# Optimization experiments

Hardware: AMD Instinct MI355X
Metric: run time of the kernel (lower is better)

The kernel has to match this reference:

```python
import jax, jax.numpy as jnp
import numpy as np

BATCH, IN_DIM, GRID, HID, DEPTH = 2048, 128, 128, 256, 7
BN_EPS = 1e-5


def setup_inputs() -> dict:
    key = jax.random.key(0)
    ks = jax.random.split(key, 10)
    x = jax.random.uniform(ks[0], (BATCH, IN_DIM), dtype=jnp.float32)
    grids = jax.random.uniform(ks[1], (DEPTH, IN_DIM, GRID), dtype=jnp.float32)  # torch.rand init
    fs = jax.random.normal(ks[2], (DEPTH, IN_DIM, GRID, HID), dtype=jnp.float32)
    depth_scores = jnp.ones((DEPTH,), dtype=jnp.float32)
    mlp_W = jax.random.normal(ks[3], (3, HID, HID), dtype=jnp.float32) * (1.0 / np.sqrt(HID))
    mlp_b = jnp.zeros((3, HID), dtype=jnp.float32)
    bn_gamma = jnp.ones((3, HID), dtype=jnp.float32)
    bn_beta = jnp.zeros((3, HID), dtype=jnp.float32)
    W_out = jax.random.normal(ks[4], (HID, 1), dtype=jnp.float32) * (1.0 / np.sqrt(HID))
    b_out = jnp.zeros((1,), dtype=jnp.float32)
    return {"x": x, "grids": grids, "fs": fs, "depth_scores": depth_scores,
            "mlp_W": mlp_W, "mlp_b": mlp_b, "bn_gamma": bn_gamma,
            "bn_beta": bn_beta, "W_out": W_out, "b_out": b_out}


def reference(x, grids, fs, depth_scores, mlp_W, mlp_b, bn_gamma, bn_beta, W_out, b_out):
    # per-feature min-max normalization over the batch dim
    xmin = x.min(axis=0, keepdims=True)
    xmax = x.max(axis=0, keepdims=True)
    z = (x - xmin) / (xmax - xmin + 1e-6)  # [B, I]

    outputs = []
    for i in range(DEPTH):
        Bmat = jax.nn.relu(z[:, :, None] - grids[i][None, :, :])  # [B, I, G]
        # (B.unsqueeze(-1) * fs[i]).sum(2).sum(1) == einsum big,igh->bh
        H = jnp.einsum('big,igh->bh', Bmat, fs[i])  # [B, H]
        if i > 0:  # residual accumulation
            H = H + outputs[-1]
        outputs.append(H)
    stacked = jnp.stack(outputs, axis=0)  # [D, B, H]
    w = jax.nn.softmax(depth_scores)  # depth attention
    h = jnp.einsum('d,dbh->bh', w, stacked)

    # MLP head (BatchNorm uses batch stats = training-mode behaviour; Dropout off)
    for j in range(3):
        h = h @ mlp_W[j] + mlp_b[j]
        mean = h.mean(axis=0)
        var = h.var(axis=0)  # biased, matching torch BN normalization
        h = (h - mean) * jax.lax.rsqrt(var + BN_EPS) * bn_gamma[j] + bn_beta[j]
        h = jax.nn.gelu(h, approximate=False)  # torch nn.GELU is exact erf GELU
    return h @ W_out + b_out
```

## Files before the change

kernel.cpp:

```cpp
#include <hip/hip_runtime.h>
#include <hip/hip_bf16.h>

#define BATCH 2048
#define IN_DIM 128
#define GRIDN 128
#define HID 256
#define DEPTH 7

typedef unsigned int u32;
typedef __attribute__((ext_vector_type(8))) short short8;
typedef __attribute__((ext_vector_type(4))) float floatx4;

#define OFF_FST   ((size_t)0)
#define SZ_FST    ((size_t)7*128*256*128*2)
#define OFF_ZT    (OFF_FST + SZ_FST)
#define SZ_ZT     ((size_t)BATCH*IN_DIM*4)
#define OFF_HPRE  (OFF_ZT + SZ_ZT)
#define SZ_HPRE   ((size_t)BATCH*HID*4)
#define OFF_STATS (OFF_HPRE + SZ_HPRE)
#define SZ_STATS  ((size_t)3*2*HID*4)
#define OFF_KEYS  (OFF_STATS + SZ_STATS)
#define SZ_KEYS   ((size_t)256*4)
#define OFF_CW    (OFF_KEYS + SZ_KEYS)
#define SZ_CW     ((size_t)32)
#define OFF_Y1    (OFF_CW + SZ_CW)
#define SZ_Y      ((size_t)BATCH*HID*4)
#define OFF_Y2    (OFF_Y1 + SZ_Y)
#define OFF_Y3    (OFF_Y2 + SZ_Y)

__device__ __forceinline__ void gload_lds16(const void* g, void* l) {
  __builtin_amdgcn_global_load_lds(
      (const __attribute__((address_space(1))) u32*)g,
      (__attribute__((address_space(3))) u32*)l, 16, 0, 0);
}

__device__ __forceinline__ u32 pack2_bf16(float lo, float hi) {
  __hip_bfloat162 b2;
  b2.x = __float2bfloat16(lo);
  b2.y = __float2bfloat16(hi);
  return *reinterpret_cast<u32*>(&b2);
}

__device__ __forceinline__ u32 pk_trunc(float a, float b) {
  return __builtin_amdgcn_perm(__float_as_uint(b), __float_as_uint(a), 0x07060302u);
}

__device__ __forceinline__ float gelu_exact(float x) {
  return 0.5f * x * (1.0f + erff(x * 0.70710678118654752f));
}

__global__ void prep1_kernel(const float* __restrict__ x, u32* __restrict__ keys,
                             const float* __restrict__ depth_scores,
                             float* __restrict__ cw) {
  int t = threadIdx.x;
  int base = blockIdx.x * 256 + t;
  float mn = 1e30f, mx = -1e30f;
#pragma unroll
  for (int j = 0; j < 16; ++j) {
    float v = x[base + j * 16384];
    mn = fminf(mn, v); mx = fmaxf(mx, v);
  }
  __shared__ float smn[256], smx[256];
  smn[t] = mn; smx[t] = mx;
  __syncthreads();
  if (t < 128) {
    mn = fminf(smn[t], smn[t + 128]);
    mx = fmaxf(smx[t], smx[t + 128]);
    int i = base & 127;
    atomicMax(&keys[i], 0x7FFFFFFFu - __float_as_uint(mn));
    atomicMax(&keys[128 + i], __float_as_uint(mx));
  }
  if (blockIdx.x == 0 && t == 0) {
    float m = -1e30f;
    for (int d0 = 0; d0 < DEPTH; ++d0) m = fmaxf(m, depth_scores[d0]);
    float e[DEPTH]; float sum = 0.f;
    for (int d0 = 0; d0 < DEPTH; ++d0) { e[d0] = expf(depth_scores[d0] - m); sum += e[d0]; }
    float cacc = 0.f; float cs[DEPTH];
    for (int d0 = DEPTH - 1; d0 >= 0; --d0) { cacc += e[d0] / sum; cs[d0] = cacc; }
    for (int d0 = 0; d0 < DEPTH; ++d0) cw[d0] = cs[d0];
  }
}

__global__ void prep2_kernel(const float* __restrict__ x, const u32* __restrict__ keys,
                             float* __restrict__ z_t) {
  __shared__ float lds[128 * 65];
  int t = threadIdx.x;
  int b0 = blockIdx.x * 64;
#pragma unroll
  for (int q = 0; q < 32; ++q) {
    int idx = q * 256 + t;
    int b = idx >> 7, i = idx & 127;
    lds[i * 65 + b] = x[(size_t)(b0 + b) * IN_DIM + i];
  }
  __syncthreads();
#pragma unroll
  for (int q = 0; q < 32; ++q) {
    int idx = q * 256 + t;
    int ii = idx >> 6, bb = idx & 63;
    float mnv = __uint_as_float(0x7FFFFFFFu - keys[ii]);
    float mxv = __uint_as_float(keys[128 + ii]);
    float v = (lds[ii * 65 + bb] - mnv) * (1.0f / (mxv - mnv + 1e-6f));
    z_t[(size_t)ii * BATCH + b0 + bb] = v;
  }
}

__global__ void convert_kernel(const float* __restrict__ fs,
                               const float* __restrict__ cw,
                               __hip_bfloat16* __restrict__ fs2) {
  __shared__ u32 lds[256 * 33];
  int slab = blockIdx.x;
  int t = threadIdx.x;
  float cd = cw[slab >> 7];
  const float* src = fs + (size_t)slab * (GRIDN * HID);
  char* dstb = (char*)fs2 + (size_t)slab * 65536;

  for (int gh = 0; gh < 2; ++gh) {
    const float* s0 = src + (size_t)gh * 64 * HID + t;
#pragma unroll
    for (int g2 = 0; g2 < 32; ++g2) {
      float va = s0[(size_t)(2 * g2) * HID];
      float vb = s0[(size_t)(2 * g2 + 1) * HID];
      lds[t * 33 + g2] = pack2_bf16(cd * va, cd * vb);
    }
    __syncthreads();
#pragma unroll
    for (int it2 = 0; it2 < 8; ++it2) {
      int task = t + it2 * 256;
      int c = task >> 9;
      int q = task & 511;
      int nhalf = c >> 1, ksl = c & 1;
      int tt = q >> 6, l4 = (q >> 4) & 3, l15 = q & 15;
      int h = nhalf * 128 + tt * 16 + l15;
      int m = ksl * 4 + l4;
      u32 a0 = lds[h * 33 + m * 4 + 0];
      u32 a1 = lds[h * 33 + m * 4 + 1];
      u32 a2 = lds[h * 33 + m * 4 + 2];
      u32 a3 = lds[h * 33 + m * 4 + 3];
      size_t off = (size_t)nhalf * 32768 + (size_t)(gh * 2 + ksl) * 8192 +
                   (size_t)tt * 1024 + l4 * 256 + l15 * 16;
      *(uint4*)(dstb + off) = make_uint4(a0, a1, a2, a3);
    }
    __syncthreads();
  }
}

#define FENCE __asm__ volatile("" ::: "memory")
#define WAITV(c) do { __builtin_amdgcn_s_waitcnt(c); FENCE; } while (0)
#define VM14 0x0F7E
#define VM4  0x0F74
#define VM0  0x0F70

__launch_bounds__(256, 2)
__global__ void gemm_kernel(const float* __restrict__ z_t,
                            const float* __restrict__ grids,
                            const __hip_bfloat16* __restrict__ fs2,
                            float* __restrict__ h_pre) {
  __shared__ __align__(16) char lds[65536];

  int bx = blockIdx.x;
  int xcd = bx & 7;
  int t6 = bx >> 3;
  int cg = t6 >> 4;
  int jb = t6 & 15;
  int chunk = xcd + 8 * cg;
  int slab0 = chunk * 28;

  int tid = threadIdx.x;
  int w = tid >> 6, l = tid & 63;
  int l15 = l & 15, l4 = l >> 4;
  int wm = w >> 1;
  int wn = w & 1;
  int mbase = jb * 128 + wm * 64;
  int nbase = wn * 128;
  char* mylds = lds + w * 16384;

  floatx4 acc[4][8];
#pragma unroll
  for (int a = 0; a < 4; ++a)
#pragma unroll
    for (int b = 0; b < 8; ++b) acc[a][b] = (floatx4)0.f;

  const char* fsb = (const char*)fs2 + (size_t)slab0 * 65536 + (size_t)wn * 32768 +
                    (size_t)l * 16;

  auto stage4 = [&](int u) {
    const char* srcb = fsb + (size_t)(u >> 3) * 65536 + (size_t)((u >> 1) & 3) * 8192 +
                       (size_t)(u & 1) * 4096;
    char* dst = mylds + (u & 3) * 4096;
#pragma unroll
    for (int j = 0; j < 4; ++j)
      gload_lds16(srcb + j * 1024, dst + j * 1024);
  };

  float4 zA, zB;
  float4 g0A, g1A, g0B, g1B;
  auto zgload = [&](int s, float4& zv, float4& G0, float4& G1) {
    int slab = slab0 + (s >> 2);
    int iz = slab & 127;
    const float* zp = z_t + (size_t)iz * BATCH + mbase + l15;
    zv.x = zp[0]; zv.y = zp[16]; zv.z = zp[32]; zv.w = zp[48];
    const float* gp = grids + (size_t)slab * GRIDN + (s & 3) * 32 + l4 * 8;
    G0 = *(const float4*)gp;
    G1 = *(const float4*)(gp + 4);
  };

  short8 af[4];
  short8 bf[4];
  auto rdfrag = [&](const int bufIdx) {
    const char* bp = mylds + bufIdx * 4096 + l * 16;
    bf[0] = *(const short8*)(bp);
    bf[1] = *(const short8*)(bp + 1024);
    bf[2] = *(const short8*)(bp + 2048);
    bf[3] = *(const short8*)(bp + 3072);
  };
  auto afgen = [&](const float4 zv, const float4 G0, const float4 G1) {
#pragma unroll
    for (int u = 0; u < 4; ++u) {
      float zu = (u == 0) ? zv.x : (u == 1) ? zv.y : (u == 2) ? zv.z : zv.w;
      union { uint4 q; short8 s8; } pk;
      pk.q.x = pk_trunc(fmaxf(zu - G0.x, 0.f), fmaxf(zu - G0.y, 0.f));
      pk.q.y = pk_trunc(fmaxf(zu - G0.z, 0.f), fmaxf(zu - G0.w, 0.f));
      pk.q.z = pk_trunc(fmaxf(zu - G1.x, 0.f), fmaxf(zu - G1.y, 0.f));
      pk.q.w = pk_trunc(fmaxf(zu - G1.z, 0.f), fmaxf(zu - G1.w, 0.f));
      af[u] = pk.s8;
    }
  };
  auto mfma16 = [&](const int ttBase) {
    __builtin_amdgcn_s_setprio(1);
#pragma unroll
    for (int u = 0; u < 4; ++u) {
      acc[u][ttBase + 0] = __builtin_amdgcn_mfma_f32_16x16x32_bf16(af[u], bf[0], acc[u][ttBase + 0], 0, 0, 0);
      acc[u][ttBase + 1] = __builtin_amdgcn_mfma_f32_16x16x32_bf16(af[u], bf[1], acc[u][ttBase + 1], 0, 0, 0);
      acc[u][ttBase + 2] = __builtin_amdgcn_mfma_f32_16x16x32_bf16(af[u], bf[2], acc[u][ttBase + 2], 0, 0, 0);
      acc[u][ttBase + 3] = __builtin_amdgcn_mfma_f32_16x16x32_bf16(af[u], bf[3], acc[u][ttBase + 3], 0, 0, 0);
    }
    __builtin_amdgcn_s_setprio(0);
  };

  zgload(0, zA, g0A, g1A); FENCE;
  stage4(0); stage4(1); stage4(2); FENCE;
  zgload(1, zB, g0B, g1B); FENCE;

#pragma unroll 1
  for (int s = 0; s < 110; s += 2) {
    WAITV(VM14);
    stage4(2 * s + 3); FENCE;
    rdfrag(0);
    afgen(zA, g0A, g1A);
    mfma16(0);
    WAITV(VM14);
    stage4(2 * s + 4); FENCE;
    zgload(s + 2, zA, g0A, g1A); FENCE;
    rdfrag(1);
    mfma16(4);
    WAITV(VM14);
    stage4(2 * s + 5); FENCE;
    rdfrag(2);
    afgen(zB, g0B, g1B);
    mfma16(0);
    WAITV(VM14);
    stage4(2 * s + 6); FENCE;
    zgload(s + 3, zB, g0B, g1B); FENCE;
    rdfrag(3);
    mfma16(4);
  }

  WAITV(VM14);
  stage4(223); FENCE;
  rdfrag(0);
  afgen(zA, g0A, g1A);
  mfma16(0);
  WAITV(VM14);
  rdfrag(1);
  mfma16(4);
  WAITV(VM4);
  rdfrag(2);
  afgen(zB, g0B, g1B);
  mfma16(0);
  WAITV(VM0);
  rdfrag(3);
  mfma16(4);

  int row0 = mbase + l4 * 4;
  int col0 = nbase + l15;
#pragma unroll
  for (int u = 0; u < 4; ++u) {
#pragma unroll
    for (int tt = 0; tt < 8; ++tt) {
      int col = col0 + tt * 16;
#pragma unroll
      for (int r = 0; r < 4; ++r) {
        int row = row0 + u * 16 + r;
        atomicAdd(&h_pre[(size_t)row * HID + col], acc[u][tt][r]);
      }
    }
  }
}

template <int FIRST>
__global__ void mlp_kernel(const float* __restrict__ Xin,
                           const float* __restrict__ statsIn,
                           const float* __restrict__ gamma,
                           const float* __restrict__ beta,
                           const float* __restrict__ W,
                           const float* __restrict__ bias,
                           float* __restrict__ Yout,
                           float* __restrict__ statsOut) {
  __shared__ float Xs[4][HID];
  int br = blockIdx.x, c = threadIdx.x;
  float mean = 0.f, rstd = 1.f, gm = 1.f, bt = 0.f;
  if (!FIRST) {
    float s1 = statsIn[c], s2 = statsIn[HID + c];
    mean = s1 * (1.0f / BATCH);
    float var = s2 * (1.0f / BATCH) - mean * mean;
    rstd = rsqrtf(var + 1e-5f);
    gm = gamma[c]; bt = beta[c];
  }
#pragma unroll
  for (int r = 0; r < 4; ++r) {
    float v = Xin[(size_t)(br * 4 + r) * HID + c];
    if (!FIRST) v = gelu_exact((v - mean) * rstd * gm + bt);
    Xs[r][c] = v;
  }
  __syncthreads();
  float acc[4] = {0, 0, 0, 0};
#pragma unroll 8
  for (int k = 0; k < HID; ++k) {
    float wv = W[(size_t)k * HID + c];
#pragma unroll
    for (int r = 0; r < 4; ++r) acc[r] += Xs[r][k] * wv;
  }
  float bb = bias[c];
  float s1 = 0.f, s2 = 0.f;
#pragma unroll
  for (int r = 0; r < 4; ++r) {
    float y = acc[r] + bb;
    Yout[(size_t)(br * 4 + r) * HID + c] = y;
    s1 += y; s2 += y * y;
  }
  atomicAdd(&statsOut[c], s1);
  atomicAdd(&statsOut[HID + c], s2);
}

__global__ void final_kernel(const float* __restrict__ Y3,
                             const float* __restrict__ statsIn,
                             const float* __restrict__ gamma,
                             const float* __restrict__ beta,
                             const float* __restrict__ W_out,
                             const float* __restrict__ b_out,
                             float* __restrict__ out) {
  int w = threadIdx.x >> 6, l = threadIdx.x & 63;
  int b = blockIdx.x * 4 + w;
  float4 y = *(const float4*)(Y3 + (size_t)b * HID + l * 4);
  float4 wv = *(const float4*)(W_out + l * 4);
  float r4[4] = {y.x, y.y, y.z, y.w};
  float w4[4] = {wv.x, wv.y, wv.z, wv.w};
  float s = 0.f;
  int c0 = l * 4;
#pragma unroll
  for (int q = 0; q < 4; ++q) {
    int c = c0 + q;
    float s1 = statsIn[c], s2 = statsIn[HID + c];
    float mean = s1 * (1.0f / BATCH);
    float var = s2 * (1.0f / BATCH) - mean * mean;
    float rstd = rsqrtf(var + 1e-5f);
    float v = gelu_exact((r4[q] - mean) * rstd * gamma[c] + beta[c]);
    s += v * w4[q];
  }
#pragma unroll
  for (int off = 32; off > 0; off >>= 1) s += __shfl_down(s, off);
  if (l == 0) out[b] = s + b_out[0];
}

extern "C" void kernel_launch(void* const* d_in, const int* in_sizes, int n_in,
                              void* d_out, int out_size, void* d_ws, size_t ws_size,
                              hipStream_t stream) {
  const float* x      = (const float*)d_in[0];
  const float* grids  = (const float*)d_in[1];
  const float* fs     = (const float*)d_in[2];
  const float* dscore = (const float*)d_in[3];
  const float* mlp_W  = (const float*)d_in[4];
  const float* mlp_b  = (const float*)d_in[5];
  const float* bn_g   = (const float*)d_in[6];
  const float* bn_b   = (const float*)d_in[7];
  const float* W_out  = (const float*)d_in[8];
  const float* b_out  = (const float*)d_in[9];
  float* out = (float*)d_out;

  char* ws = (char*)d_ws;
  __hip_bfloat16* fs2 = (__hip_bfloat16*)(ws + OFF_FST);
  float* z_t   = (float*)(ws + OFF_ZT);
  float* h_pre = (float*)(ws + OFF_HPRE);
  float* stats = (float*)(ws + OFF_STATS);
  u32*   keys  = (u32*)(ws + OFF_KEYS);
  float* cw    = (float*)(ws + OFF_CW);
  float* Y1    = (float*)(ws + OFF_Y1);
  float* Y2    = (float*)(ws + OFF_Y2);
  float* Y3    = (float*)(ws + OFF_Y3);

  hipMemsetAsync(h_pre, 0, SZ_HPRE + SZ_STATS + SZ_KEYS, stream);

  prep1_kernel<<<64, 256, 0, stream>>>(x, keys, dscore, cw);
  prep2_kernel<<<32, 256, 0, stream>>>(x, keys, z_t);
  convert_kernel<<<DEPTH * IN_DIM, 256, 0, stream>>>(fs, cw, fs2);
  gemm_kernel<<<512, 256, 0, stream>>>(z_t, grids, fs2, h_pre);

  mlp_kernel<1><<<512, 256, 0, stream>>>(h_pre, nullptr, nullptr, nullptr,
                                         mlp_W, mlp_b, Y1, stats);
  mlp_kernel<0><<<512, 256, 0, stream>>>(Y1, stats, bn_g, bn_b,
                                         mlp_W + 65536, mlp_b + 256, Y2, stats + 512);
  mlp_kernel<0><<<512, 256, 0, stream>>>(Y2, stats + 512, bn_g + 256, bn_b + 256,
                                         mlp_W + 2 * 65536, mlp_b + 2 * 256, Y3, stats + 1024);
  final_kernel<<<512, 256, 0, stream>>>(Y3, stats + 1024, bn_g + 512, bn_b + 512,
                                        W_out, b_out, out);
}
```

Measured before the change: 439.5 us.

## Share fs tile staging across waves with block barriers and reduce LDS

```diff
diff --git a/kernel.cpp b/kernel.cpp
--- a/kernel.cpp
+++ b/kernel.cpp
@@ -43,6 +43,10 @@
 
 __device__ __forceinline__ u32 pk_trunc(float a, float b) {
   return __builtin_amdgcn_perm(__float_as_uint(b), __float_as_uint(a), 0x07060302u);
+}
+
+__device__ __forceinline__ float reluc(float v) {
+  return __builtin_amdgcn_fmed3f(v, 0.0f, 1.0f);
 }
 
 __device__ __forceinline__ float gelu_exact(float x) {
@@ -146,33 +150,33 @@
 
 #define FENCE __asm__ volatile("" ::: "memory")
 #define WAITV(c) do { __builtin_amdgcn_s_waitcnt(c); FENCE; } while (0)
-#define VM14 0x0F7E
-#define VM4  0x0F74
-#define VM0  0x0F70
+#define BARR do { FENCE; __builtin_amdgcn_s_barrier(); FENCE; } while (0)
+#define VM8 0x0F78
+#define VM1 0x0F71
+#define VM0 0x0F70
 
 __launch_bounds__(256, 2)
 __global__ void gemm_kernel(const float* __restrict__ z_t,
                             const float* __restrict__ grids,
                             const __hip_bfloat16* __restrict__ fs2,
                             float* __restrict__ h_pre) {
-  __shared__ __align__(16) char lds[65536];
+  __shared__ __align__(16) char lds[16384];
 
   int bx = blockIdx.x;
   int xcd = bx & 7;
   int t6 = bx >> 3;
   int cg = t6 >> 4;
-  int jb = t6 & 15;
+  int jb2 = t6 & 15;
   int chunk = xcd + 8 * cg;
   int slab0 = chunk * 28;
+  int mt = jb2 >> 1;
+  int nh = jb2 & 1;
 
   int tid = threadIdx.x;
   int w = tid >> 6, l = tid & 63;
   int l15 = l & 15, l4 = l >> 4;
-  int wm = w >> 1;
-  int wn = w & 1;
-  int mbase = jb * 128 + wm * 64;
-  int nbase = wn * 128;
-  char* mylds = lds + w * 16384;
+  int mbase = mt * 256 + w * 64;
+  int nbase = nh * 128;
 
   floatx4 acc[4][8];
 #pragma unroll
@@ -180,16 +184,13 @@
 #pragma unroll
     for (int b = 0; b < 8; ++b) acc[a][b] = (floatx4)0.f;
 
-  const char* fsb = (const char*)fs2 + (size_t)slab0 * 65536 + (size_t)wn * 32768 +
-                    (size_t)l * 16;
-
-  auto stage4 = [&](int u) {
+  const char* fsb = (const char*)fs2 + (size_t)slab0 * 65536 + (size_t)nh * 32768 +
+                    (size_t)w * 1024 + (size_t)l * 16;
+
+  auto stage1 = [&](int u) {
     const char* srcb = fsb + (size_t)(u >> 3) * 65536 + (size_t)((u >> 1) & 3) * 8192 +
                        (size_t)(u & 1) * 4096;
-    char* dst = mylds + (u & 3) * 4096;
-#pragma unroll
-    for (int j = 0; j < 4; ++j)
-      gload_lds16(srcb + j * 1024, dst + j * 1024);
+    gload_lds16(srcb, lds + (u & 3) * 4096 + w * 1024);
   };
 
   float4 zA, zB;
@@ -207,7 +208,7 @@
   short8 af[4];
   short8 bf[4];
   auto rdfrag = [&](const int bufIdx) {
-    const char* bp = mylds + bufIdx * 4096 + l * 16;
+    const char* bp = lds + bufIdx * 4096 + l * 16;
     bf[0] = *(const short8*)(bp);
     bf[1] = *(const short8*)(bp + 1024);
     bf[2] = *(const short8*)(bp + 2048);
@@ -218,10 +219,10 @@
     for (int u = 0; u < 4; ++u) {
       float zu = (u == 0) ? zv.x : (u == 1) ? zv.y : (u == 2) ? zv.z : zv.w;
       union { uint4 q; short8 s8; } pk;
-      pk.q.x = pk_trunc(fmaxf(zu - G0.x, 0.f), fmaxf(zu - G0.y, 0.f));
-      pk.q.y = pk_trunc(fmaxf(zu - G0.z, 0.f), fmaxf(zu - G0.w, 0.f));
-      pk.q.z = pk_trunc(fmaxf(zu - G1.x, 0.f), fmaxf(zu - G1.y, 0.f));
-      pk.q.w = pk_trunc(fmaxf(zu - G1.z, 0.f), fmaxf(zu - G1.w, 0.f));
+      pk.q.x = pk_trunc(reluc(zu - G0.x), reluc(zu - G0.y));
+      pk.q.y = pk_trunc(reluc(zu - G0.z), reluc(zu - G0.w));
+      pk.q.z = pk_trunc(reluc(zu - G1.x), reluc(zu - G1.y));
+      pk.q.w = pk_trunc(reluc(zu - G1.z), reluc(zu - G1.w));
       af[u] = pk.s8;
     }
   };
@@ -238,46 +239,46 @@
   };
 
   zgload(0, zA, g0A, g1A); FENCE;
-  stage4(0); stage4(1); stage4(2); FENCE;
+  stage1(0); stage1(1); stage1(2); FENCE;
   zgload(1, zB, g0B, g1B); FENCE;
 
 #pragma unroll 1
   for (int s = 0; s < 110; s += 2) {
-    WAITV(VM14);
-    stage4(2 * s + 3); FENCE;
+    WAITV(VM8); BARR;
+    stage1(2 * s + 3); FENCE;
+    afgen(zA, g0A, g1A);
     rdfrag(0);
-    afgen(zA, g0A, g1A);
     mfma16(0);
-    WAITV(VM14);
-    stage4(2 * s + 4); FENCE;
+    WAITV(VM8); BARR;
+    stage1(2 * s + 4); FENCE;
     zgload(s + 2, zA, g0A, g1A); FENCE;
     rdfrag(1);
     mfma16(4);
-    WAITV(VM14);
-    stage4(2 * s + 5); FENCE;
+    WAITV(VM8); BARR;
+    stage1(2 * s + 5); FENCE;
+    afgen(zB, g0B, g1B);
     rdfrag(2);
-    afgen(zB, g0B, g1B);
     mfma16(0);
-    WAITV(VM14);
-    stage4(2 * s + 6); FENCE;
+    WAITV(VM8); BARR;
+    stage1(2 * s + 6); FENCE;
     zgload(s + 3, zB, g0B, g1B); FENCE;
     rdfrag(3);
     mfma16(4);
   }
 
-  WAITV(VM14);
-  stage4(223); FENCE;
+  WAITV(VM8); BARR;
+  stage1(223); FENCE;
+  afgen(zA, g0A, g1A);
   rdfrag(0);
-  afgen(zA, g0A, g1A);
   mfma16(0);
-  WAITV(VM14);
+  WAITV(VM8); BARR;
   rdfrag(1);
   mfma16(4);
-  WAITV(VM4);
+  WAITV(VM1); BARR;
+  afgen(zB, g0B, g1B);
   rdfrag(2);
-  afgen(zB, g0B, g1B);
   mfma16(0);
-  WAITV(VM0);
+  WAITV(VM0); BARR;
   rdfrag(3);
   mfma16(4);
 
```

Measured after the change: 429.0 us. -2.4%, faster.
